# Performance work log

Hardware: AMD Instinct MI355X
Metric: run time of the kernel (lower is better)

## Reference

```python
import jax, jax.numpy as jnp
from jax import lax
import numpy as np

B, C, H, W = 32, 3, 224, 224
NUM_CLASSES = 100
K = 3  # kernel size
OUT1 = 32


def _bn(x, g, b, m, v, eps=1e-5):
    # eval-mode batchnorm over channel dim of NCHW
    inv = g / jnp.sqrt(v + eps)
    return x * inv[None, :, None, None] + (b - m * inv)[None, :, None, None]


def _conv(x, w, pad=1):
    return lax.conv_general_dilated(
        x, w, (1, 1), ((pad, pad), (pad, pad)),
        dimension_numbers=('NCHW', 'OIHW', 'NCHW'))


def _maxpool2(x):
    return lax.reduce_window(x, -jnp.inf, lax.max, (1, 1, 2, 2), (1, 1, 2, 2), 'VALID')


def setup_inputs() -> dict:
    key = jax.random.key(0)
    ks = jax.random.split(key, 32)
    n = lambda k, s, sc=0.05: jax.random.normal(k, s, jnp.float32) * sc
    u = lambda k, s: jax.random.uniform(k, s, jnp.float32, 0.5, 1.5)
    inp = {
        'x': jax.random.normal(ks[0], (B, C, H, W), jnp.float32),
        # weight_gen MLP: Linear(3,128)->ReLU->Linear(128,256)->ReLU->Linear(256, 32*3*3*3)
        'w1': n(ks[1], (128, C)), 'b1': n(ks[2], (128,)),
        'w2': n(ks[3], (256, 128)), 'b2': n(ks[4], (256,)),
        'w3': n(ks[5], (OUT1 * C * K * K, 256)), 'b3': n(ks[6], (OUT1 * C * K * K,)),
        # bias_gen: Linear(3, 32)
        'wb': n(ks[7], (OUT1, C)), 'bb': n(ks[8], (OUT1,)),
        'conv2_w': n(ks[9], (64, 32, 3, 3)), 'conv2_b': n(ks[10], (64,)),
        'conv3_w': n(ks[11], (128, 64, 3, 3)), 'conv3_b': n(ks[12], (128,)),
        'bn1_g': 1.0 + n(ks[13], (32,)), 'bn1_b': n(ks[14], (32,)), 'bn1_m': n(ks[15], (32,)), 'bn1_v': u(ks[16], (32,)),
        'bn2_g': 1.0 + n(ks[17], (64,)), 'bn2_b': n(ks[18], (64,)), 'bn2_m': n(ks[19], (64,)), 'bn2_v': u(ks[20], (64,)),
        'bn3_g': 1.0 + n(ks[21], (128,)), 'bn3_b': n(ks[22], (128,)), 'bn3_m': n(ks[23], (128,)), 'bn3_v': u(ks[24], (128,)),
        'fc_w': n(ks[25], (NUM_CLASSES, 128)), 'fc_b': n(ks[26], (NUM_CLASSES,)),
    }
    return inp


def reference(x, w1, b1, w2, b2, w3, b3, wb, bb, conv2_w, conv2_b, conv3_w, conv3_b,
              bn1_g, bn1_b, bn1_m, bn1_v, bn2_g, bn2_b, bn2_m, bn2_v,
              bn3_g, bn3_b, bn3_m, bn3_v, fc_w, fc_b):
    Bx = x.shape[0]
    # DynamicConv2D: channel indicator is all-ones since C == max_in_channels
    ind = jnp.ones((Bx, C), x.dtype)
    h = jax.nn.relu(ind @ w1.T + b1)
    h = jax.nn.relu(h @ w2.T + b2)
    dyn_w = (h @ w3.T + b3).reshape(Bx, OUT1, C, K, K)  # per-sample [O,I,k,k]
    dyn_b = ind @ wb.T + bb                             # per-sample [O]
    # vmap over batch: one single-image conv per sample with its own weights
    y = jax.vmap(lambda xi, wi, bi: _conv(xi[None], wi)[0] + bi[:, None, None])(x, dyn_w, dyn_b)
    y = jax.nn.relu(_bn(y, bn1_g, bn1_b, bn1_m, bn1_v))
    y = _maxpool2(y)
    y = jax.nn.relu(_bn(_conv(y, conv2_w) + conv2_b[None, :, None, None], bn2_g, bn2_b, bn2_m, bn2_v))
    y = _maxpool2(y)
    y = jax.nn.relu(_bn(_conv(y, conv3_w) + conv3_b[None, :, None, None], bn3_g, bn3_b, bn3_m, bn3_v))
    y = y.mean(axis=(2, 3))  # AdaptiveAvgPool2d((1,1)) + flatten
    # dropout is identity in eval
    return y @ fc_w.T + fc_b
```

## Files before the change

kernel.cpp:

```cpp
#include <hip/hip_runtime.h>
#include <hip/hip_bf16.h>

#define BATCH 32
#define HW1 224

typedef __attribute__((ext_vector_type(8))) short short8;
typedef __attribute__((ext_vector_type(4))) float floatx4;

static __device__ __forceinline__ unsigned short f2bf(float f) {
    unsigned int u = __float_as_uint(f);
    unsigned int r = (u + 0x7fffu + ((u >> 16) & 1u)) >> 16;
    return (unsigned short)r;
}

typedef __attribute__((address_space(1))) const unsigned int guint;
typedef __attribute__((address_space(3))) unsigned int suint;
static __device__ __forceinline__ void gload_lds16(const void* g, void* l) {
    __builtin_amdgcn_global_load_lds((guint*)g, (suint*)l, 16, 0, 0);
}

#define MFMA(A, B, C) __builtin_amdgcn_mfma_f32_16x16x32_bf16((A), (B), (C), 0, 0, 0)

__global__ __launch_bounds__(256) void gen_dynw_repack(
    const float* __restrict__ w1, const float* __restrict__ b1,
    const float* __restrict__ w2, const float* __restrict__ b2,
    const float* __restrict__ w3, const float* __restrict__ b3,
    const float* __restrict__ conv2_w, const float* __restrict__ conv3_w,
    const float* __restrict__ wb, const float* __restrict__ bb,
    const float* __restrict__ conv2_b, const float* __restrict__ conv3_b,
    const float* __restrict__ bn1_g, const float* __restrict__ bn1_b,
    const float* __restrict__ bn1_m, const float* __restrict__ bn1_v,
    const float* __restrict__ bn2_g, const float* __restrict__ bn2_b,
    const float* __restrict__ bn2_m, const float* __restrict__ bn2_v,
    const float* __restrict__ bn3_g, const float* __restrict__ bn3_b,
    const float* __restrict__ bn3_m, const float* __restrict__ bn3_v,
    unsigned short* __restrict__ swpre,
    unsigned short* __restrict__ wrep2, unsigned short* __restrict__ wrep3,
    float* __restrict__ bn1_s, float* __restrict__ bn1_t,
    float* __restrict__ bn2_s, float* __restrict__ bn2_t,
    float* __restrict__ bn3_s, float* __restrict__ bn3_t,
    float* __restrict__ feat)
{
    __shared__ float h1s[128];
    __shared__ float h2s[256];
    const int blk = blockIdx.x;
    const int t = threadIdx.x;
    if (blk < 216) {
        if (t < 128) {
            float s = b1[t] + w1[t*3+0] + w1[t*3+1] + w1[t*3+2];
            h1s[t] = fmaxf(s, 0.f);
        }
        __syncthreads();
        {
            float s0 = b2[t], s1 = 0.f, s2 = 0.f, s3 = 0.f;
            const float* wr = w2 + (size_t)t*128;
#pragma unroll 4
            for (int k = 0; k < 128; k += 4) {
                float4 wv = *(const float4*)(wr + k);
                s0 = fmaf(wv.x, h1s[k  ], s0);
                s1 = fmaf(wv.y, h1s[k+1], s1);
                s2 = fmaf(wv.z, h1s[k+2], s2);
                s3 = fmaf(wv.w, h1s[k+3], s3);
            }
            h2s[t] = fmaxf((s0 + s1) + (s2 + s3), 0.f);
        }
        __syncthreads();
        const int wave = t >> 6, lane = t & 63;
        const int row = blk*4 + wave;
        float4 wv = *(const float4*)(w3 + (size_t)row*256 + lane*4);
        float4 hv = *(const float4*)&h2s[lane*4];
        float s = wv.x*hv.x + wv.y*hv.y + wv.z*hv.z + wv.w*hv.w;
#pragma unroll
        for (int m = 1; m < 64; m <<= 1) s += __shfl_xor(s, m);
        if (lane == 0) {
            int oc = row / 27, tap = row - oc*27;
            int ic = tap / 9, kk = tap - ic*9;
            int ky = kk / 3, kx = kk - ky*3;
            unsigned short v = f2bf(s + b3[row]);
            int pos;
            if (kk == 8)      pos = 1024 + oc*32 + ic;
            else if (kx < 2)  pos = oc*32 + ky*8 + kx*4 + ic;
            else              pos = oc*32 + 24 + ky*4 + ic;
            swpre[pos] = v;
        }
    } else if (blk < 576) {
        const int i = (blk - 216)*256 + t;
        const int N2 = 9*64*32;
        if (i < N2) {
            int tp = i / (64*32); int rem = i - tp*(64*32);
            int oc = rem >> 5, ic = rem & 31;
            wrep2[i] = f2bf(conv2_w[(oc*32 + ic)*9 + tp]);
        } else {
            int j = i - N2;
            int tp = j / (128*64); int rem = j - tp*(128*64);
            int oc = rem >> 6, ic = rem & 63;
            wrep3[j] = f2bf(conv3_w[(oc*64 + ic)*9 + tp]);
        }
    } else {
        if (t < 32) {
            float dynb = bb[t] + wb[t*3+0] + wb[t*3+1] + wb[t*3+2];
            float s = bn1_g[t] / sqrtf(bn1_v[t] + 1e-5f);
            bn1_s[t] = s;
            bn1_t[t] = (dynb - bn1_m[t]) * s + bn1_b[t];
        }
        if (t < 64) {
            float s = bn2_g[t] / sqrtf(bn2_v[t] + 1e-5f);
            bn2_s[t] = s;
            bn2_t[t] = (conv2_b[t] - bn2_m[t]) * s + bn2_b[t];
        }
        if (t < 128) {
            float s = bn3_g[t] / sqrtf(bn3_v[t] + 1e-5f);
            bn3_s[t] = s;
            bn3_t[t] = (conv3_b[t] - bn3_m[t]) * s + bn3_b[t];
        }
        for (int i = t; i < BATCH*128; i += 256) feat[i] = 0.f;
    }
}

__global__ __launch_bounds__(256) void conv1_pool(
    const float* __restrict__ x,
    const unsigned short* __restrict__ swpre,
    const float* __restrict__ bn_s, const float* __restrict__ bn_t,
    unsigned short* __restrict__ act1)
{
    __shared__ __align__(16) unsigned short sp[18*20*4];
    __shared__ __align__(16) unsigned short swAB[2048];

    const int tid = threadIdx.x;
    const int bx = blockIdx.x, by = blockIdx.y, b = blockIdx.z;
    const int gy0 = by*16 - 1;
    const int gxs0 = bx*16 - 2;
    const float* xb = x + (size_t)b * 3 * HW1 * HW1;

    {
        uint4 w = *(const uint4*)(swpre + tid*8);
        if (tid < 128) {
            w.y &= 0xFFFFu; w.w &= 0xFFFFu;
        } else if (((tid*8) & 31) != 0) {
            w.x = 0u; w.y = 0u; w.z = 0u; w.w = 0u;
        } else {
            w.y &= 0xFFFFu; w.z = 0u; w.w = 0u;
        }
        *(uint4*)&swAB[tid*8] = w;
    }

    float2 c0 = {0.f, 0.f}, c1 = {0.f, 0.f}, c2 = {0.f, 0.f};
    if (tid < 180) {
        int row = tid / 10, p = tid - row*10;
        int gy = gy0 + row, gx = gxs0 + p*2;
        if (((unsigned)gy < HW1) && ((unsigned)gx <= 222u)) {
            const float* pp = xb + gy*HW1 + gx;
            c0 = *(const float2*)(pp);
            c1 = *(const float2*)(pp + HW1*HW1);
            c2 = *(const float2*)(pp + 2*HW1*HW1);
        }
        uint4 v;
        v.x = (unsigned int)f2bf(c0.x) | ((unsigned int)f2bf(c1.x) << 16);
        v.y = (unsigned int)f2bf(c2.x);
        v.z = (unsigned int)f2bf(c0.y) | ((unsigned int)f2bf(c1.y) << 16);
        v.w = (unsigned int)f2bf(c2.y);
        *(uint4*)&sp[tid*8] = v;
    }
    __syncthreads();

    const int lane = tid & 63, wave = tid >> 6;
    const int n = lane & 15, quad = lane >> 4;

    short8 afrA[2], afrB[2];
#pragma unroll
    for (int h = 0; h < 2; ++h) {
        afrA[h] = *(const short8*)&swAB[((h*16 + n)*32) + quad*8];
        afrB[h] = *(const short8*)&swAB[1024 + ((h*16 + n)*32) + quad*8];
    }
    float4 sv[2], tv[2];
#pragma unroll
    for (int h = 0; h < 2; ++h) {
        sv[h] = *(const float4*)(bn_s + h*16 + quad*4);
        tv[h] = *(const float4*)(bn_t + h*16 + quad*4);
    }

    union U { short8 s8; uint2 u2[2]; };

    const int y0w = wave*4;
    float ev[2][4];

#pragma unroll
    for (int yi = 0; yi < 4; ++yi) {
        const int y = y0w + yi;
        int r0 = (quad < 3) ? (y + quad) : y;
        int c0i = (quad < 3) ? n : (n + 2);
        int r1 = (quad < 3) ? (y + quad) : (y + 1);
        int c1i = (quad < 3) ? (n + 1) : (n + 2);
        U bf1;
        bf1.u2[0] = *(const uint2*)&sp[(r0*20 + c0i + 1)*4];
        bf1.u2[1] = *(const uint2*)&sp[(r1*20 + c1i + 1)*4];
        U bf2;
        bf2.u2[0] = *(const uint2*)&sp[((y+2)*20 + (n+3))*4];
        bf2.u2[1] = bf2.u2[0];

        float vr[2][4];
#pragma unroll
        for (int h = 0; h < 2; ++h) {
            floatx4 acc = {0.f, 0.f, 0.f, 0.f};
            acc = MFMA(afrA[h], bf1.s8, acc);
            acc = MFMA(afrB[h], bf2.s8, acc);
            float sj[4] = {sv[h].x, sv[h].y, sv[h].z, sv[h].w};
            float tj[4] = {tv[h].x, tv[h].y, tv[h].z, tv[h].w};
#pragma unroll
            for (int j = 0; j < 4; ++j)
                vr[h][j] = fmaxf(fmaf(acc[j], sj[j], tj[j]), 0.f);
        }

        if ((yi & 1) == 0) {
#pragma unroll
            for (int h = 0; h < 2; ++h)
#pragma unroll
                for (int j = 0; j < 4; ++j) ev[h][j] = vr[h][j];
        } else {
            int py = by*8 + ((y0w + yi) >> 1);
            int px = bx*8 + (n >> 1);
            unsigned short* dstp =
                act1 + ((size_t)((b*112 + py)*112 + px))*32 + quad*4;
#pragma unroll
            for (int h = 0; h < 2; ++h) {
                unsigned int pk[2];
#pragma unroll
                for (int j = 0; j < 4; ++j) {
                    float m = fmaxf(vr[h][j], ev[h][j]);
                    m = fmaxf(m, __shfl_xor(m, 1));
                    unsigned short us = f2bf(m);
                    if (j & 1) pk[j >> 1] |= ((unsigned int)us) << 16;
                    else       pk[j >> 1]  = us;
                }
                if (!(n & 1)) *(uint2*)(dstp + h*16) = *(uint2*)pk;
            }
        }
    }
}

__global__ __launch_bounds__(256) void conv2_mfma(
    const unsigned short* __restrict__ act1,
    const unsigned short* __restrict__ wrep,
    const float* __restrict__ bn_s, const float* __restrict__ bn_t,
    unsigned short* __restrict__ act2)
{
    constexpr int IC = 32, OC = 64, H = 112;
    __shared__ __align__(16) short lds[4*18*18*8];

    const int tid = threadIdx.x;
    const int b = blockIdx.z;
    const int cx0 = blockIdx.x*16, cy0 = blockIdx.y*16;
    const unsigned short* ab = act1 + (size_t)b*H*H*IC;

    unsigned bad = 0;
    {
        int k = 0;
        for (int s = tid; s < 4*324; s += 256, ++k) {
            int ck = s / 324; int rem = s - ck*324;
            int y = rem / 18, xx = rem - y*18;
            int gy = cy0 - 1 + y, gx = cx0 - 1 + xx;
            if (!(((unsigned)gy < H) && ((unsigned)gx < H))) {
                bad |= 1u << k; gy = 0; gx = 0;
            }
            gload_lds16(ab + (size_t)(gy*H + gx)*IC + ck*8, &lds[s*8]);
        }
        if (bad) {
            asm volatile("s_waitcnt vmcnt(0)" ::: "memory");
            k = 0;
            for (int s = tid; s < 4*324; s += 256, ++k)
                if (bad & (1u << k)) {
                    uint4 z = {0u,0u,0u,0u};
                    *(uint4*)&lds[s*8] = z;
                }
        }
    }

    const int lane = tid & 63, wave = tid >> 6;
    const int n = lane & 15, quad = lane >> 4;
    const int oc0w = wave * 16;

    short8 afr[9];
#pragma unroll
    for (int t = 0; t < 9; ++t)
        afr[t] = *(const short8*)(wrep + (size_t)(t*OC + oc0w + n)*IC + quad*8);

    float4 sv = *(const float4*)(bn_s + oc0w + quad*4);
    float4 tv = *(const float4*)(bn_t + oc0w + quad*4);
    float sj[4] = {sv.x, sv.y, sv.z, sv.w};
    float tj[4] = {tv.x, tv.y, tv.z, tv.w};

    __syncthreads();

    floatx4 acc[3];
    float ev[4];

#pragma unroll
    for (int r = 0; r < 18; ++r) {
        const short* rp = &lds[((quad*18 + r)*18 + n)*8];
        short8 w0 = *(const short8*)(rp);
        short8 w1 = *(const short8*)(rp + 8);
        short8 w2 = *(const short8*)(rp + 16);

        if (r < 16) {
            floatx4 a = {0.f,0.f,0.f,0.f};
            a = MFMA(afr[0], w0, a);
            a = MFMA(afr[1], w1, a);
            a = MFMA(afr[2], w2, a);
            acc[r % 3] = a;
        }
        if (r >= 1 && r <= 16) {
            int y = r - 1;
            floatx4 a = acc[y % 3];
            a = MFMA(afr[3], w0, a);
            a = MFMA(afr[4], w1, a);
            a = MFMA(afr[5], w2, a);
            acc[y % 3] = a;
        }
        if (r >= 2) {
            int y = r - 2;
            floatx4 a = acc[y % 3];
            a = MFMA(afr[6], w0, a);
            a = MFMA(afr[7], w1, a);
            a = MFMA(afr[8], w2, a);

            float v[4];
#pragma unroll
            for (int j = 0; j < 4; ++j)
                v[j] = fmaxf(fmaf(a[j], sj[j], tj[j]), 0.f);

            if ((y & 1) == 0) {
#pragma unroll
                for (int j = 0; j < 4; ++j) ev[j] = v[j];
            } else {
                unsigned int pk[2];
#pragma unroll
                for (int j = 0; j < 4; ++j) {
                    float m = fmaxf(v[j], ev[j]);
                    m = fmaxf(m, __shfl_xor(m, 1));
                    unsigned short us = f2bf(m);
                    if (j & 1) pk[j >> 1] |= ((unsigned int)us) << 16;
                    else       pk[j >> 1]  = us;
                }
                if (!(n & 1)) {
                    int py = (cy0 >> 1) + (y >> 1), px = (cx0 >> 1) + (n >> 1);
                    unsigned short* dstp =
                        act2 + ((size_t)((b*56 + py)*56 + px))*OC + oc0w + quad*4;
                    *(uint2*)dstp = *(uint2*)pk;
                }
            }
        }
    }
}

__global__ __launch_bounds__(256) void conv3_mfma(
    const unsigned short* __restrict__ act2,
    const unsigned short* __restrict__ wrep,
    const float* __restrict__ bn_s, const float* __restrict__ bn_t,
    float* __restrict__ feat)
{
    constexpr int IC = 64, OC = 128, H = 56;
    __shared__ __align__(16) short lds[8*16*18*8];

    const int tid = threadIdx.x;
    const int b = blockIdx.z >> 1, half = blockIdx.z & 1;
    const int cx0 = blockIdx.x*16, cy0 = blockIdx.y*14;
    const unsigned short* ab = act2 + (size_t)b*H*H*IC;

    unsigned bad = 0;
    {
        int k = 0;
        for (int s = tid; s < 8*16*18; s += 256, ++k) {
            int ck = s / (16*18); int rem = s - ck*(16*18);
            int y = rem / 18, xx = rem - y*18;
            int gy = cy0 - 1 + y, gx = cx0 - 1 + xx;
            if (!(((unsigned)gy < H) && ((unsigned)gx < H))) {
                bad |= 1u << k; gy = 0; gx = 0;
            }
            gload_lds16(ab + (size_t)(gy*H + gx)*IC + ck*8, &lds[s*8]);
        }
        if (bad) {
            asm volatile("s_waitcnt vmcnt(0)" ::: "memory");
            k = 0;
            for (int s = tid; s < 8*16*18; s += 256, ++k)
                if (bad & (1u << k)) {
                    uint4 z = {0u,0u,0u,0u};
                    *(uint4*)&lds[s*8] = z;
                }
        }
    }

    const int lane = tid & 63, wave = tid >> 6;
    const int n = lane & 15, quad = lane >> 4;
    const int oc0w = half*64 + wave*16;

    short8 afr[18];
#pragma unroll
    for (int t = 0; t < 9; ++t)
#pragma unroll
        for (int kc = 0; kc < 2; ++kc)
            afr[t*2 + kc] = *(const short8*)(wrep + (size_t)(t*OC + oc0w + n)*IC + kc*32 + quad*8);

    float4 sv = *(const float4*)(bn_s + oc0w + quad*4);
    float4 tv = *(const float4*)(bn_t + oc0w + quad*4);
    float sj[4] = {sv.x, sv.y, sv.z, sv.w};
    float tj[4] = {tv.x, tv.y, tv.z, tv.w};

    __syncthreads();

    float sum[4] = {0.f, 0.f, 0.f, 0.f};
    const bool vx = (cx0 + n) < H;
    floatx4 acc[3];

#pragma unroll
    for (int r = 0; r < 16; ++r) {
        const short* p0 = &lds[((quad*16     + r)*18 + n)*8];
        const short* p1 = &lds[(((4+quad)*16 + r)*18 + n)*8];
        short8 a0 = *(const short8*)(p0);
        short8 a1 = *(const short8*)(p0 + 8);
        short8 a2 = *(const short8*)(p0 + 16);
        short8 b0 = *(const short8*)(p1);
        short8 b1 = *(const short8*)(p1 + 8);
        short8 b2 = *(const short8*)(p1 + 16);

        if (r < 14) {
            floatx4 a = {0.f,0.f,0.f,0.f};
            a = MFMA(afr[0], a0, a);
            a = MFMA(afr[1], b0, a);
            a = MFMA(afr[2], a1, a);
            a = MFMA(afr[3], b1, a);
            a = MFMA(afr[4], a2, a);
            a = MFMA(afr[5], b2, a);
            acc[r % 3] = a;
        }
        if (r >= 1 && r <= 14) {
            int y = r - 1;
            floatx4 a = acc[y % 3];
            a = MFMA(afr[6],  a0, a);
            a = MFMA(afr[7],  b0, a);
            a = MFMA(afr[8],  a1, a);
            a = MFMA(afr[9],  b1, a);
            a = MFMA(afr[10], a2, a);
            a = MFMA(afr[11], b2, a);
            acc[y % 3] = a;
        }
        if (r >= 2) {
            int y = r - 2;
            floatx4 a = acc[y % 3];
            a = MFMA(afr[12], a0, a);
            a = MFMA(afr[13], b0, a);
            a = MFMA(afr[14], a1, a);
            a = MFMA(afr[15], b1, a);
            a = MFMA(afr[16], a2, a);
            a = MFMA(afr[17], b2, a);
            if (vx) {
#pragma unroll
                for (int j = 0; j < 4; ++j)
                    sum[j] += fmaxf(fmaf(a[j], sj[j], tj[j]), 0.f);
            }
        }
    }
#pragma unroll
    for (int j = 0; j < 4; ++j) {
        sum[j] += __shfl_xor(sum[j], 1);
        sum[j] += __shfl_xor(sum[j], 2);
        sum[j] += __shfl_xor(sum[j], 4);
        sum[j] += __shfl_xor(sum[j], 8);
    }
    if (n == 0) {
#pragma unroll
        for (int j = 0; j < 4; ++j)
            atomicAdd(&feat[b*128 + oc0w + quad*4 + j], sum[j]);
    }
}

__global__ __launch_bounds__(256) void fc_kernel(
    const float* __restrict__ feat, const float* __restrict__ fc_w,
    const float* __restrict__ fc_b, float* __restrict__ out)
{
    int g = blockIdx.x * 16 + (threadIdx.x >> 4);
    int l = threadIdx.x & 15;
    if (g >= BATCH*100) return;
    int b = g / 100, n = g - b*100;
    const float* f = feat + b*128 + l*8;
    const float* w = fc_w + (size_t)n*128 + l*8;
    float4 f0 = *(const float4*)(f);
    float4 f1 = *(const float4*)(f + 4);
    float4 w0 = *(const float4*)(w);
    float4 w1 = *(const float4*)(w + 4);
    float s = f0.x*w0.x + f0.y*w0.y + f0.z*w0.z + f0.w*w0.w
            + f1.x*w1.x + f1.y*w1.y + f1.z*w1.z + f1.w*w1.w;
    s += __shfl_xor(s, 1);
    s += __shfl_xor(s, 2);
    s += __shfl_xor(s, 4);
    s += __shfl_xor(s, 8);
    if (l == 0) out[g] = s * (1.f/3136.f) + fc_b[n];
}

extern "C" void kernel_launch(void* const* d_in, const int* in_sizes, int n_in,
                              void* d_out, int out_size, void* d_ws, size_t ws_size,
                              hipStream_t stream)
{
    const float* x       = (const float*)d_in[0];
    const float* w1      = (const float*)d_in[1];
    const float* b1      = (const float*)d_in[2];
    const float* w2      = (const float*)d_in[3];
    const float* b2      = (const float*)d_in[4];
    const float* w3      = (const float*)d_in[5];
    const float* b3      = (const float*)d_in[6];
    const float* wb      = (const float*)d_in[7];
    const float* bb      = (const float*)d_in[8];
    const float* conv2_w = (const float*)d_in[9];
    const float* conv2_b = (const float*)d_in[10];
    const float* conv3_w = (const float*)d_in[11];
    const float* conv3_b = (const float*)d_in[12];
    const float* bn1_g = (const float*)d_in[13];
    const float* bn1_b = (const float*)d_in[14];
    const float* bn1_m = (const float*)d_in[15];
    const float* bn1_v = (const float*)d_in[16];
    const float* bn2_g = (const float*)d_in[17];
    const float* bn2_b = (const float*)d_in[18];
    const float* bn2_m = (const float*)d_in[19];
    const float* bn2_v = (const float*)d_in[20];
    const float* bn3_g = (const float*)d_in[21];
    const float* bn3_b = (const float*)d_in[22];
    const float* bn3_m = (const float*)d_in[23];
    const float* bn3_v = (const float*)d_in[24];
    const float* fc_w  = (const float*)d_in[25];
    const float* fc_b  = (const float*)d_in[26];
    float* out = (float*)d_out;

    char* wsb = (char*)d_ws;
    float* ws    = (float*)d_ws;
    float* bn1_s = ws + 864;
    float* bn1_t = ws + 896;
    float* bn2_s = ws + 928;
    float* bn2_t = ws + 992;
    float* bn3_s = ws + 1056;
    float* bn3_t = ws + 1184;
    float* feat  = ws + 1312;
    unsigned short* swpre = (unsigned short*)(wsb + 24576);
    unsigned short* wrep2 = (unsigned short*)(wsb + 32768);
    unsigned short* wrep3 = (unsigned short*)(wsb + 69632);
    unsigned short* act1  = (unsigned short*)(wsb + 262144);
    unsigned short* act2  = (unsigned short*)(wsb + 262144 + 25690112);

    gen_dynw_repack<<<577, 256, 0, stream>>>(
        w1, b1, w2, b2, w3, b3, conv2_w, conv3_w,
        wb, bb, conv2_b, conv3_b,
        bn1_g, bn1_b, bn1_m, bn1_v, bn2_g, bn2_b, bn2_m, bn2_v,
        bn3_g, bn3_b, bn3_m, bn3_v,
        swpre, wrep2, wrep3,
        bn1_s, bn1_t, bn2_s, bn2_t, bn3_s, bn3_t, feat);

    conv1_pool<<<dim3(14, 14, BATCH), 256, 0, stream>>>(
        x, swpre, bn1_s, bn1_t, act1);

    conv2_mfma<<<dim3(7, 7, BATCH), 256, 0, stream>>>(
        act1, wrep2, bn2_s, bn2_t, act2);

    conv3_mfma<<<dim3(4, 4, BATCH*2), 256, 0, stream>>>(
        act2, wrep3, bn3_s, bn3_t, feat);

    fc_kernel<<<200, 256, 0, stream>>>(feat, fc_w, fc_b, out);
}
```

Measured before the change: 181.2 us.

## Fold weight repack into conv1 and fuse FC into conv3 via last-block counter

Moves the conv2/conv3 weight repacking out of the generator kernel and into the first 360 blocks of conv1_pool, so the generator launch shrinks to 217 blocks. Removes the separate FC kernel: conv3 blocks bump a global counter after their atomic feature accumulation, and the last block to finish computes the FC layer from features staged in LDS. This saves one kernel launch and some serialization between small kernels. In exchange, the FC layer runs on a single block, and every block pays a threadfence plus an atomic.

Measured after the change: 284.9 us. 1.57x slower.

```diff
diff --git a/kernel.cpp b/kernel.cpp
--- a/kernel.cpp
+++ b/kernel.cpp
@@ -21,11 +21,10 @@
 
 #define MFMA(A, B, C) __builtin_amdgcn_mfma_f32_16x16x32_bf16((A), (B), (C), 0, 0, 0)
 
-__global__ __launch_bounds__(256) void gen_dynw_repack(
+__global__ __launch_bounds__(256) void gen_dynw(
     const float* __restrict__ w1, const float* __restrict__ b1,
     const float* __restrict__ w2, const float* __restrict__ b2,
     const float* __restrict__ w3, const float* __restrict__ b3,
-    const float* __restrict__ conv2_w, const float* __restrict__ conv3_w,
     const float* __restrict__ wb, const float* __restrict__ bb,
     const float* __restrict__ conv2_b, const float* __restrict__ conv3_b,
     const float* __restrict__ bn1_g, const float* __restrict__ bn1_b,
@@ -35,11 +34,10 @@
     const float* __restrict__ bn3_g, const float* __restrict__ bn3_b,
     const float* __restrict__ bn3_m, const float* __restrict__ bn3_v,
     unsigned short* __restrict__ swpre,
-    unsigned short* __restrict__ wrep2, unsigned short* __restrict__ wrep3,
     float* __restrict__ bn1_s, float* __restrict__ bn1_t,
     float* __restrict__ bn2_s, float* __restrict__ bn2_t,
     float* __restrict__ bn3_s, float* __restrict__ bn3_t,
-    float* __restrict__ feat)
+    float* __restrict__ feat, int* __restrict__ cnt)
 {
     __shared__ float h1s[128];
     __shared__ float h2s[256];
@@ -83,19 +81,6 @@
             else              pos = oc*32 + 24 + ky*4 + ic;
             swpre[pos] = v;
         }
-    } else if (blk < 576) {
-        const int i = (blk - 216)*256 + t;
-        const int N2 = 9*64*32;
-        if (i < N2) {
-            int tp = i / (64*32); int rem = i - tp*(64*32);
-            int oc = rem >> 5, ic = rem & 31;
-            wrep2[i] = f2bf(conv2_w[(oc*32 + ic)*9 + tp]);
-        } else {
-            int j = i - N2;
-            int tp = j / (128*64); int rem = j - tp*(128*64);
-            int oc = rem >> 6, ic = rem & 63;
-            wrep3[j] = f2bf(conv3_w[(oc*64 + ic)*9 + tp]);
-        }
     } else {
         if (t < 32) {
             float dynb = bb[t] + wb[t*3+0] + wb[t*3+1] + wb[t*3+2];
@@ -114,12 +99,15 @@
             bn3_t[t] = (conv3_b[t] - bn3_m[t]) * s + bn3_b[t];
         }
         for (int i = t; i < BATCH*128; i += 256) feat[i] = 0.f;
+        if (t == 0) *cnt = 0;
     }
 }
 
 __global__ __launch_bounds__(256) void conv1_pool(
     const float* __restrict__ x,
     const unsigned short* __restrict__ swpre,
+    const float* __restrict__ conv2_w, const float* __restrict__ conv3_w,
+    unsigned short* __restrict__ wrep2, unsigned short* __restrict__ wrep3,
     const float* __restrict__ bn_s, const float* __restrict__ bn_t,
     unsigned short* __restrict__ act1)
 {
@@ -128,6 +116,25 @@
 
     const int tid = threadIdx.x;
     const int bx = blockIdx.x, by = blockIdx.y, b = blockIdx.z;
+
+    {
+        int flat = (b*14 + by)*14 + bx;
+        if (flat < 360) {
+            int i = flat*256 + tid;
+            const int N2 = 9*64*32;
+            if (i < N2) {
+                int tp = i / (64*32); int rem = i - tp*(64*32);
+                int oc = rem >> 5, ic = rem & 31;
+                wrep2[i] = f2bf(conv2_w[(oc*32 + ic)*9 + tp]);
+            } else {
+                int j = i - N2;
+                int tp = j / (128*64); int rem = j - tp*(128*64);
+                int oc = rem >> 6, ic = rem & 63;
+                wrep3[j] = f2bf(conv3_w[(oc*64 + ic)*9 + tp]);
+            }
+        }
+    }
+
     const int gy0 = by*16 - 1;
     const int gxs0 = bx*16 - 2;
     const float* xb = x + (size_t)b * 3 * HW1 * HW1;
@@ -352,14 +359,17 @@
     }
 }
 
-__global__ __launch_bounds__(256) void conv3_mfma(
+__global__ __launch_bounds__(256) void conv3_mfma_fc(
     const unsigned short* __restrict__ act2,
     const unsigned short* __restrict__ wrep,
     const float* __restrict__ bn_s, const float* __restrict__ bn_t,
-    float* __restrict__ feat)
+    float* __restrict__ feat, int* __restrict__ cnt,
+    const float* __restrict__ fc_w, const float* __restrict__ fc_b,
+    float* __restrict__ out)
 {
     constexpr int IC = 64, OC = 128, H = 56;
     __shared__ __align__(16) short lds[8*16*18*8];
+    __shared__ int lastflag;
 
     const int tid = threadIdx.x;
     const int b = blockIdx.z >> 1, half = blockIdx.z & 1;
@@ -471,29 +481,32 @@
         for (int j = 0; j < 4; ++j)
             atomicAdd(&feat[b*128 + oc0w + quad*4 + j], sum[j]);
     }
-}
-
-__global__ __launch_bounds__(256) void fc_kernel(
-    const float* __restrict__ feat, const float* __restrict__ fc_w,
-    const float* __restrict__ fc_b, float* __restrict__ out)
-{
-    int g = blockIdx.x * 16 + (threadIdx.x >> 4);
-    int l = threadIdx.x & 15;
-    if (g >= BATCH*100) return;
-    int b = g / 100, n = g - b*100;
-    const float* f = feat + b*128 + l*8;
-    const float* w = fc_w + (size_t)n*128 + l*8;
-    float4 f0 = *(const float4*)(f);
-    float4 f1 = *(const float4*)(f + 4);
-    float4 w0 = *(const float4*)(w);
-    float4 w1 = *(const float4*)(w + 4);
-    float s = f0.x*w0.x + f0.y*w0.y + f0.z*w0.z + f0.w*w0.w
-            + f1.x*w1.x + f1.y*w1.y + f1.z*w1.z + f1.w*w1.w;
-    s += __shfl_xor(s, 1);
-    s += __shfl_xor(s, 2);
-    s += __shfl_xor(s, 4);
-    s += __shfl_xor(s, 8);
-    if (l == 0) out[g] = s * (1.f/3136.f) + fc_b[n];
+
+    __threadfence();
+    __syncthreads();
+    if (tid == 0) lastflag = (atomicAdd(cnt, 1) == 4*4*BATCH*2 - 1) ? 1 : 0;
+    __syncthreads();
+    if (lastflag) {
+        float* lfeat = (float*)lds;
+        for (int i = tid; i < BATCH*128; i += 256)
+            lfeat[i] = atomicAdd(&feat[i], 0.f);
+        __syncthreads();
+        for (int g = tid; g < BATCH*100; g += 256) {
+            int bb2 = g / 100, nn = g - bb2*100;
+            const float* fw = fc_w + (size_t)nn*128;
+            const float* fl = lfeat + bb2*128;
+            float s = 0.f;
+#pragma unroll 4
+            for (int k = 0; k < 128; k += 4) {
+                float4 wv = *(const float4*)(fw + k);
+                s = fmaf(fl[k  ], wv.x, s);
+                s = fmaf(fl[k+1], wv.y, s);
+                s = fmaf(fl[k+2], wv.z, s);
+                s = fmaf(fl[k+3], wv.w, s);
+            }
+            out[g] = s * (1.f/3136.f) + fc_b[nn];
+        }
+    }
 }
 
 extern "C" void kernel_launch(void* const* d_in, const int* in_sizes, int n_in,
@@ -538,28 +551,27 @@
     float* bn3_s = ws + 1056;
     float* bn3_t = ws + 1184;
     float* feat  = ws + 1312;
+    int*   cnt   = (int*)(wsb + 22016);
     unsigned short* swpre = (unsigned short*)(wsb + 24576);
     unsigned short* wrep2 = (unsigned short*)(wsb + 32768);
     unsigned short* wrep3 = (unsigned short*)(wsb + 69632);
     unsigned short* act1  = (unsigned short*)(wsb + 262144);
     unsigned short* act2  = (unsigned short*)(wsb + 262144 + 25690112);
 
-    gen_dynw_repack<<<577, 256, 0, stream>>>(
-        w1, b1, w2, b2, w3, b3, conv2_w, conv3_w,
+    gen_dynw<<<217, 256, 0, stream>>>(
+        w1, b1, w2, b2, w3, b3,
         wb, bb, conv2_b, conv3_b,
         bn1_g, bn1_b, bn1_m, bn1_v, bn2_g, bn2_b, bn2_m, bn2_v,
         bn3_g, bn3_b, bn3_m, bn3_v,
-        swpre, wrep2, wrep3,
-        bn1_s, bn1_t, bn2_s, bn2_t, bn3_s, bn3_t, feat);
+        swpre,
+        bn1_s, bn1_t, bn2_s, bn2_t, bn3_s, bn3_t, feat, cnt);
 
     conv1_pool<<<dim3(14, 14, BATCH), 256, 0, stream>>>(
-        x, swpre, bn1_s, bn1_t, act1);
+        x, swpre, conv2_w, conv3_w, wrep2, wrep3, bn1_s, bn1_t, act1);
 
     conv2_mfma<<<dim3(7, 7, BATCH), 256, 0, stream>>>(
         act1, wrep2, bn2_s, bn2_t, act2);
 
-    conv3_mfma<<<dim3(4, 4, BATCH*2), 256, 0, stream>>>(
-        act2, wrep3, bn3_s, bn3_t, feat);
-
-    fc_kernel<<<200, 256, 0, stream>>>(feat, fc_w, fc_b, out);
-}
+    conv3_mfma_fc<<<dim3(4, 4, BATCH*2), 256, 0, stream>>>(
+        act2, wrep3, bn3_s, bn3_t, feat, cnt, fc_w, fc_b, out);
+}
```
